# Kernel tuning notes

Hardware: AMD Instinct MI355X
Metric: run time of the kernel (lower is better)

Reference implementation:

```python
import jax, jax.numpy as jnp
import numpy as np

B, N, S, D = 8, 8192, 4, 256


def setup_inputs() -> dict:
    key = jax.random.key(0)
    kx, kj, kk, k1, k2, k3, k4 = jax.random.split(key, 7)
    x = jax.random.normal(kx, (B, N, D), dtype=jnp.float32)
    ji = jax.random.randint(kj, (B, N, S), 0, N, dtype=jnp.int64)
    ki = jax.random.randint(kk, (B, N, S), 0, N, dtype=jnp.int64)
    # params of nn.Sequential(Linear(3D, D), GELU, Linear(D, D))
    W1 = jax.random.normal(k1, (3 * D, D), dtype=jnp.float32) * 0.02
    b1 = jax.random.normal(k2, (D,), dtype=jnp.float32) * 0.02
    W2 = jax.random.normal(k3, (D, D), dtype=jnp.float32) * 0.02
    b2 = jax.random.normal(k4, (D,), dtype=jnp.float32) * 0.02
    return {"x": x, "ji": ji, "ki": ki, "W1": W1, "b1": b1, "W2": W2, "b2": b2}


def reference(x, ji, ki, W1, b1, W2, b2):
    # gather neighbor features per batch element: [B,N,S,D]
    gather = jax.vmap(lambda xb, ib: xb[ib])
    xj = gather(x, ji)
    xk = gather(x, ki)
    xi = jnp.broadcast_to(x[:, :, None, :], (B, N, S, D))
    h = jnp.concatenate([xi, xj, xk], axis=-1)            # [B,N,S,3D]
    h = jax.nn.gelu(jnp.einsum('bnse,ed->bnsd', h, W1) + b1, approximate=False)
    out = jnp.einsum('bnse,ed->bnsd', h, W2) + b2         # [B,N,S,D]
    return out.mean(axis=2)                               # [B,N,D]
```

## Files before the change

kernel.cpp:

```cpp
#include <hip/hip_runtime.h>
#include <hip/hip_bf16.h>

#define Bb 8
#define Nn 8192
#define Ss 4
#define Dd 256
#define MTOT (Bb*Nn)

typedef unsigned short u16;
typedef short short8 __attribute__((ext_vector_type(8)));
typedef unsigned short u16x4 __attribute__((ext_vector_type(4)));
typedef float f32x4 __attribute__((ext_vector_type(4)));

static __device__ __forceinline__ float bf2f(u16 v) {
  union { unsigned int u; float f; } x; x.u = ((unsigned int)v) << 16; return x.f;
}
static __device__ __forceinline__ u16 f2bf(float f) {
  union { float f; unsigned int u; } x; x.f = f;
  unsigned int u = x.u;
  return (u16)((u + 0x7fffu + ((u >> 16) & 1u)) >> 16);
}

static __device__ __forceinline__ float gelu_fast(float x) {
  float x2 = x * x;
  float z = x * (-2.3021277f - 0.10294456f * x2);
  float e = __builtin_amdgcn_exp2f(z);
  return x * __builtin_amdgcn_rcpf(1.0f + e);
}

__global__ __launch_bounds__(256) void prep_kernel(
    const float* __restrict__ x, const float* __restrict__ W1,
    const float* __restrict__ W2,
    u16* __restrict__ xb, u16* __restrict__ W1t, u16* __restrict__ W2t)
{
  int bid = blockIdx.x, t = threadIdx.x;
  if (bid < 16384) {
    size_t i = ((size_t)bid * 256 + t) * 4;
    f32x4 v = *(const f32x4*)&x[i];
    u16x4 o;
    o[0] = f2bf(v[0]); o[1] = f2bf(v[1]); o[2] = f2bf(v[2]); o[3] = f2bf(v[3]);
    *(u16x4*)&xb[i] = o;
  } else if (bid < 16384 + 768) {
    int j = (bid - 16384) * 256 + t;
    int n = j >> 8, k = j & 255;
    int tb = n >> 8, d = n & 255;
    W1t[j] = f2bf(W1[(size_t)(tb * 256 + k) * 256 + d]);
  } else {
    int j = (bid - 17152) * 256 + t;
    int n = j >> 8, k = j & 255;
    W2t[j] = f2bf(W2[(size_t)k * 256 + n]);
  }
}

template<int NBLK>
__global__ __launch_bounds__(256) void gemm128(
    const u16* __restrict__ Ag, const u16* __restrict__ Btg,
    u16* __restrict__ Out, int ldOut)
{
  __shared__ u16 As[128 * 64];
  __shared__ u16 Bs[128 * 64];
  const int t = threadIdx.x;
  const int w = t >> 6, lane = t & 63;
  const int wm = (w >> 1) * 64, wn = (w & 1) * 64;
  const int lr = lane & 15;
  const int lk = (lane >> 4) * 8;

  const int cpx = gridDim.x >> 3;
  const int bid = blockIdx.x;
  const int swz = (bid & 7) * cpx + (bid >> 3);
  const int n0 = (swz % NBLK) * 128;
  const size_t m0 = (size_t)(swz / NBLK) * 128;

  f32x4 acc[4][4];
#pragma unroll
  for (int m = 0; m < 4; ++m)
#pragma unroll
    for (int n = 0; n < 4; ++n)
      acc[m][n] = (f32x4){0.f, 0.f, 0.f, 0.f};

  for (int kt = 0; kt < 4; ++kt) {
#pragma unroll
    for (int pass = 0; pass < 4; ++pass) {
      int c = pass * 256 + t;
      int row = c >> 3, cc = c & 7;
      int scc = cc ^ (row & 7);
      const u16* ga = Ag + (m0 + row) * 256 + kt * 64 + scc * 8;
      u16* la = As + pass * 2048 + (t & 192) * 8;
      __builtin_amdgcn_global_load_lds(
          (const __attribute__((address_space(1))) void*)ga,
          (__attribute__((address_space(3))) void*)la, 16, 0, 0);
      const u16* gb = Btg + (size_t)(n0 + row) * 256 + kt * 64 + scc * 8;
      u16* lb = Bs + pass * 2048 + (t & 192) * 8;
      __builtin_amdgcn_global_load_lds(
          (const __attribute__((address_space(1))) void*)gb,
          (__attribute__((address_space(3))) void*)lb, 16, 0, 0);
    }
    __syncthreads();
#pragma unroll
    for (int kk = 0; kk < 2; ++kk) {
      short8 af[4], bfr[4];
#pragma unroll
      for (int m = 0; m < 4; ++m) {
        int rA = wm + m * 16 + lr;
        af[m] = *(const short8*)&As[(rA * 64 + kk * 32 + lk) ^ ((rA & 7) << 3)];
      }
#pragma unroll
      for (int n = 0; n < 4; ++n) {
        int rB = wn + n * 16 + lr;
        bfr[n] = *(const short8*)&Bs[(rB * 64 + kk * 32 + lk) ^ ((rB & 7) << 3)];
      }
#pragma unroll
      for (int m = 0; m < 4; ++m)
#pragma unroll
        for (int n = 0; n < 4; ++n)
          acc[m][n] = __builtin_amdgcn_mfma_f32_16x16x32_bf16(
              af[m], bfr[n], acc[m][n], 0, 0, 0);
    }
    __syncthreads();
  }

#pragma unroll
  for (int m = 0; m < 4; ++m) {
    int rbase = wm + m * 16 + ((lane >> 4) << 2);
#pragma unroll
    for (int n = 0; n < 4; ++n) {
      int col = n0 + wn + n * 16 + (lane & 15);
#pragma unroll
      for (int rr = 0; rr < 4; ++rr) {
        size_t row = m0 + rbase + rr;
        Out[row * (size_t)ldOut + col] = f2bf(acc[m][n][rr]);
      }
    }
  }
}

__global__ __launch_bounds__(256) void gather_gemm2(
    const u16* __restrict__ ABC, const int* __restrict__ ji,
    const int* __restrict__ ki, const float* __restrict__ b1,
    const u16* __restrict__ W2t, const float* __restrict__ b2,
    float* __restrict__ out)
{
  __shared__ u16 Hs[64 * 256];
  __shared__ u16 W2s[256 * 64];
  const int t = threadIdx.x;
  const int w = t >> 6, lane = t & 63;
  const size_t r0 = (size_t)blockIdx.x * 64;
  const int base = ((int)(r0 >> 13)) << 13;
  const int d0 = lane * 4;

#pragma unroll
  for (int pass = 0; pass < 8; ++pass) {
    int c = pass * 256 + t;
    int n = c >> 3, cc = c & 7;
    int scc = cc ^ (n & 7);
    const u16* g = W2t + n * 256 + scc * 8;
    u16* l = W2s + pass * 2048 + (t & 192) * 8;
    __builtin_amdgcn_global_load_lds(
        (const __attribute__((address_space(1))) void*)g,
        (__attribute__((address_space(3))) void*)l, 16, 0, 0);
  }

  f32x4 bias = *(const f32x4*)&b1[d0];
  for (int it = 0; it < 16; ++it) {
    int row = w * 16 + it;
    size_t r = r0 + row;
    u16x4 av = *(const u16x4*)(ABC + r * 768 + d0);
    float a0 = bf2f(av[0]) + bias[0];
    float a1 = bf2f(av[1]) + bias[1];
    float a2 = bf2f(av[2]) + bias[2];
    float a3 = bf2f(av[3]) + bias[3];
    const int* jr = ji + r * 4;
    const int* kr = ki + r * 4;
    float acc0 = 0.f, acc1 = 0.f, acc2 = 0.f, acc3 = 0.f;
#pragma unroll
    for (int s = 0; s < 4; ++s) {
      size_t gj = (size_t)(base + jr[s]);
      size_t gk = (size_t)(base + kr[s]);
      u16x4 bv = *(const u16x4*)(ABC + gj * 768 + 256 + d0);
      u16x4 cv = *(const u16x4*)(ABC + gk * 768 + 512 + d0);
      float x0 = a0 + bf2f(bv[0]) + bf2f(cv[0]);
      float x1 = a1 + bf2f(bv[1]) + bf2f(cv[1]);
      float x2 = a2 + bf2f(bv[2]) + bf2f(cv[2]);
      float x3 = a3 + bf2f(bv[3]) + bf2f(cv[3]);
      acc0 += gelu_fast(x0);
      acc1 += gelu_fast(x1);
      acc2 += gelu_fast(x2);
      acc3 += gelu_fast(x3);
    }
    u16x4 hv;
    hv[0] = f2bf(acc0 * 0.25f);
    hv[1] = f2bf(acc1 * 0.25f);
    hv[2] = f2bf(acc2 * 0.25f);
    hv[3] = f2bf(acc3 * 0.25f);
    *(u16x4*)&Hs[(row * 256 + d0) ^ ((row & 7) << 3)] = hv;
  }
  __syncthreads();

  const int wm = (w >> 1) * 32, wn = (w & 1) * 128;
  const int lr = lane & 15, lk = (lane >> 4) * 8;
  f32x4 acc[2][8];
#pragma unroll
  for (int m = 0; m < 2; ++m)
#pragma unroll
    for (int n = 0; n < 8; ++n)
      acc[m][n] = (f32x4){0.f, 0.f, 0.f, 0.f};

  for (int kt = 0; kt < 4; ++kt) {
#pragma unroll
    for (int kk = 0; kk < 2; ++kk) {
      short8 af[2], bfr[8];
#pragma unroll
      for (int m = 0; m < 2; ++m) {
        int rA = wm + m * 16 + lr;
        af[m] = *(const short8*)&Hs[(rA * 256 + kt * 64 + kk * 32 + lk) ^ ((rA & 7) << 3)];
      }
#pragma unroll
      for (int n = 0; n < 8; ++n) {
        int rB = wn + n * 16 + lr;
        bfr[n] = *(const short8*)&W2s[(rB * 64 + kk * 32 + lk) ^ ((rB & 7) << 3)];
      }
#pragma unroll
      for (int m = 0; m < 2; ++m)
#pragma unroll
        for (int n = 0; n < 8; ++n)
          acc[m][n] = __builtin_amdgcn_mfma_f32_16x16x32_bf16(
              af[m], bfr[n], acc[m][n], 0, 0, 0);
    }
    __syncthreads();
    if (kt < 3) {
#pragma unroll
      for (int pass = 0; pass < 8; ++pass) {
        int c = pass * 256 + t;
        int n = c >> 3, cc = c & 7;
        int scc = cc ^ (n & 7);
        const u16* g = W2t + n * 256 + (kt + 1) * 64 + scc * 8;
        u16* l = W2s + pass * 2048 + (t & 192) * 8;
        __builtin_amdgcn_global_load_lds(
            (const __attribute__((address_space(1))) void*)g,
            (__attribute__((address_space(3))) void*)l, 16, 0, 0);
      }
      __syncthreads();
    }
  }

#pragma unroll
  for (int m = 0; m < 2; ++m) {
    int rbase = wm + m * 16 + ((lane >> 4) << 2);
#pragma unroll
    for (int n = 0; n < 8; ++n) {
      int col = wn + n * 16 + lr;
      float bb = b2[col];
#pragma unroll
      for (int rr = 0; rr < 4; ++rr) {
        size_t row = r0 + rbase + rr;
        out[row * 256 + col] = acc[m][n][rr] + bb;
      }
    }
  }
}

extern "C" void kernel_launch(void* const* d_in, const int* in_sizes, int n_in,
                              void* d_out, int out_size, void* d_ws, size_t ws_size,
                              hipStream_t stream) {
  (void)in_sizes; (void)n_in; (void)out_size; (void)ws_size;
  const float* x  = (const float*)d_in[0];
  const int*   ji = (const int*)d_in[1];
  const int*   ki = (const int*)d_in[2];
  const float* W1 = (const float*)d_in[3];
  const float* b1 = (const float*)d_in[4];
  const float* W2 = (const float*)d_in[5];
  const float* b2 = (const float*)d_in[6];
  float* out = (float*)d_out;

  char* ws = (char*)d_ws;
  u16* xb  = (u16*)ws;  ws += (size_t)MTOT * 256 * 2;
  u16* ABC = (u16*)ws;  ws += (size_t)MTOT * 768 * 2;
  u16* W1t = (u16*)ws;  ws += 768 * 256 * 2;
  u16* W2t = (u16*)ws;  ws += 256 * 256 * 2;

  prep_kernel<<<17408, 256, 0, stream>>>(x, W1, W2, xb, W1t, W2t);

  gemm128<6><<<(MTOT / 128) * 6, 256, 0, stream>>>(xb, W1t, ABC, 768);

  gather_gemm2<<<MTOT / 64, 256, 0, stream>>>(ABC, ji, ki, b1, W2t, b2, out);
}
```

Baseline: 119.6 us.

## Read W2 fragments directly from global memory and swizzle block order

The second GEMM kernel no longer stages W2 tiles through shared memory with per-k-tile barriers. Each wave now loads its B fragments straight from global (L2-cached) memory inside the MFMA loop. Block indices are remapped so consecutive blocks spread across the 8 batch slices, and launch bounds request 4 blocks per CU. The goal is to remove LDS traffic and synchronisation and raise occupancy. The cost is more global/L2 load latency on the MFMA critical path.

Result: slower. 123.0 us (+2.9%).

```diff
diff --git a/kernel.cpp b/kernel.cpp
--- a/kernel.cpp
+++ b/kernel.cpp
@@ -134,31 +134,22 @@
   }
 }
 
-__global__ __launch_bounds__(256) void gather_gemm2(
+__global__ __launch_bounds__(256, 4) void gather_gemm2(
     const u16* __restrict__ ABC, const int* __restrict__ ji,
     const int* __restrict__ ki, const float* __restrict__ b1,
     const u16* __restrict__ W2t, const float* __restrict__ b2,
     float* __restrict__ out)
 {
   __shared__ u16 Hs[64 * 256];
-  __shared__ u16 W2s[256 * 64];
   const int t = threadIdx.x;
   const int w = t >> 6, lane = t & 63;
-  const size_t r0 = (size_t)blockIdx.x * 64;
+
+  const int cpx = gridDim.x >> 3;
+  const int bid = blockIdx.x;
+  const int swz = (bid & 7) * cpx + (bid >> 3);
+  const size_t r0 = (size_t)swz * 64;
   const int base = ((int)(r0 >> 13)) << 13;
   const int d0 = lane * 4;
-
-#pragma unroll
-  for (int pass = 0; pass < 8; ++pass) {
-    int c = pass * 256 + t;
-    int n = c >> 3, cc = c & 7;
-    int scc = cc ^ (n & 7);
-    const u16* g = W2t + n * 256 + scc * 8;
-    u16* l = W2s + pass * 2048 + (t & 192) * 8;
-    __builtin_amdgcn_global_load_lds(
-        (const __attribute__((address_space(1))) void*)g,
-        (__attribute__((address_space(3))) void*)l, 16, 0, 0);
-  }
 
   f32x4 bias = *(const f32x4*)&b1[d0];
   for (int it = 0; it < 16; ++it) {
@@ -205,41 +196,26 @@
     for (int n = 0; n < 8; ++n)
       acc[m][n] = (f32x4){0.f, 0.f, 0.f, 0.f};
 
+#pragma unroll
   for (int kt = 0; kt < 4; ++kt) {
 #pragma unroll
     for (int kk = 0; kk < 2; ++kk) {
-      short8 af[2], bfr[8];
+      int koff = kt * 64 + kk * 32 + lk;
+      short8 af[2];
 #pragma unroll
       for (int m = 0; m < 2; ++m) {
         int rA = wm + m * 16 + lr;
-        af[m] = *(const short8*)&Hs[(rA * 256 + kt * 64 + kk * 32 + lk) ^ ((rA & 7) << 3)];
+        af[m] = *(const short8*)&Hs[(rA * 256 + koff) ^ ((rA & 7) << 3)];
       }
 #pragma unroll
       for (int n = 0; n < 8; ++n) {
         int rB = wn + n * 16 + lr;
-        bfr[n] = *(const short8*)&W2s[(rB * 64 + kk * 32 + lk) ^ ((rB & 7) << 3)];
-      }
-#pragma unroll
-      for (int m = 0; m < 2; ++m)
-#pragma unroll
-        for (int n = 0; n < 8; ++n)
-          acc[m][n] = __builtin_amdgcn_mfma_f32_16x16x32_bf16(
-              af[m], bfr[n], acc[m][n], 0, 0, 0);
-    }
-    __syncthreads();
-    if (kt < 3) {
-#pragma unroll
-      for (int pass = 0; pass < 8; ++pass) {
-        int c = pass * 256 + t;
-        int n = c >> 3, cc = c & 7;
-        int scc = cc ^ (n & 7);
-        const u16* g = W2t + n * 256 + (kt + 1) * 64 + scc * 8;
-        u16* l = W2s + pass * 2048 + (t & 192) * 8;
-        __builtin_amdgcn_global_load_lds(
-            (const __attribute__((address_space(1))) void*)g,
-            (__attribute__((address_space(3))) void*)l, 16, 0, 0);
-      }
-      __syncthreads();
+        short8 bfr = *(const short8*)&W2t[rB * 256 + koff];
+        acc[0][n] = __builtin_amdgcn_mfma_f32_16x16x32_bf16(
+            af[0], bfr, acc[0][n], 0, 0, 0);
+        acc[1][n] = __builtin_amdgcn_mfma_f32_16x16x32_bf16(
+            af[1], bfr, acc[1][n], 0, 0, 0);
+      }
     }
   }
 
```
